# Optimization experiments

Measured on AMD Instinct MI355X. Metric: run time of the kernel, lower is better.

## Reference

```python
import jax, jax.numpy as jnp
import numpy as np

EMB = 256
N_NODES = 100000
N_EDGES = 500000
N_REL = 10
REL_DIM = 64
HID = 128
HEADS = 4
HEAD_DIM = HID // HEADS


def setup_inputs() -> dict:
    key = jax.random.key(0)
    ks = jax.random.split(key, 16)
    s = lambda i, shape: jax.random.normal(ks[i], shape, dtype=jnp.float32) * 0.05
    return {
        "node_embeddings": jax.random.normal(ks[0], (N_NODES, EMB), dtype=jnp.float32),
        "edge_index": jax.random.randint(ks[1], (2, N_EDGES), 0, N_NODES),
        "relation_type": jax.random.randint(ks[2], (N_EDGES,), 0, N_REL),
        "rel_emb": s(3, (N_REL, REL_DIM)),
        "W_edge": s(4, (2 * EMB, HID)), "b_edge": jnp.zeros((HID,), jnp.float32),
        "W_q": s(5, (REL_DIM, HID)), "b_q": jnp.zeros((HID,), jnp.float32),
        "W_k": s(6, (HID, HID)), "b_k": jnp.zeros((HID,), jnp.float32),
        "W_v": s(7, (HID, HID)), "b_v": jnp.zeros((HID,), jnp.float32),
        "W_o1": s(8, (HID, HID)), "b_o1": jnp.zeros((HID,), jnp.float32),
        "W_o2": s(9, (HID, 1)), "b_o2": jnp.zeros((1,), jnp.float32),
    }


def reference(node_embeddings, edge_index, relation_type, rel_emb,
              W_edge, b_edge, W_q, b_q, W_k, b_k, W_v, b_v,
              W_o1, b_o1, W_o2, b_o2):
    # Gather endpoint features: [E, 2*EMB]
    src = node_embeddings[edge_index[0]]
    tgt = node_embeddings[edge_index[1]]
    edge_features = jnp.concatenate([src, tgt], axis=1)
    # Edge MLP (dropout is identity at eval): [E, HID]
    edge_hidden = jax.nn.relu(edge_features @ W_edge + b_edge)
    # Relation embedding lookup: [E, REL_DIM]
    rel = rel_emb[relation_type]
    E = edge_hidden.shape[0]
    Q = (rel @ W_q + b_q).reshape(E, HEADS, HEAD_DIM)
    K = (edge_hidden @ W_k + b_k).reshape(E, HEADS, HEAD_DIM)
    V = (edge_hidden @ W_v + b_v).reshape(E, HEADS, HEAD_DIM)
    scale = jnp.sqrt(jnp.float32(HEAD_DIM))
    scores = jnp.sum(Q * K, axis=-1) / scale          # [E, HEADS]
    attn = jax.nn.softmax(scores, axis=-1)            # softmax over heads
    attended = (attn[..., None] * V).reshape(E, HID)
    output = attended + edge_hidden
    # Output MLP: Linear->ReLU->Linear(1)
    h = jax.nn.relu(output @ W_o1 + b_o1)
    score = (h @ W_o2 + b_o2).squeeze(-1)             # [E]
    return score
```

## Files before the change

kernel.cpp:

```cpp
#include <hip/hip_runtime.h>

#define EMB   256
#define HID   128
#define RELD  64
#define NREL  10
#define TE    64

typedef __attribute__((ext_vector_type(8)))  short bf16x8;
typedef __attribute__((ext_vector_type(16))) float f32x16;

__device__ __forceinline__ float bf16_to_f32(unsigned short u) {
    union { unsigned int i; float f; } v;
    v.i = ((unsigned int)u) << 16;
    return v.f;
}

__device__ __forceinline__ unsigned short f32_to_bf16(float x) {
    union { unsigned int i; float f; } v;
    v.f = x;
    unsigned int b = v.i;
    unsigned int rounded = b + 0x7fffu + ((b >> 16) & 1u);
    return (unsigned short)(rounded >> 16);
}

template <bool F32>
__device__ __forceinline__ float ldx(const void* p, size_t i) {
    if (F32) return ((const float*)p)[i];
    return bf16_to_f32(((const unsigned short*)p)[i]);
}

__device__ __forceinline__ bool detect_f32(const void* nodeEmb) {
    const float* f = (const float*)nodeEmb;
    float x = f[(threadIdx.x & 63) * 997];
    bool sane = isfinite(x) && fabsf(x) < 1.0e6f;
    unsigned long long m = __ballot(sane);
    return __popcll(m) >= 48;
}

template <bool F32>
__device__ void prep_body(const void* W_edge, const void* W_k, const void* W_v,
                          const void* W_o1, const void* rel_emb, const void* W_q,
                          const void* b_q,
                          unsigned short* WTe, unsigned short* WTk,
                          unsigned short* WTv, unsigned short* WTo1, float* Qtab)
{
    if (blockIdx.x < 448) {
        int idx = blockIdx.x * 256 + threadIdx.x;
        if (idx < 65536) {
            int col = idx >> 9, k = idx & 511;
            WTe[idx] = f32_to_bf16(ldx<F32>(W_edge, (size_t)k * HID + col));
        } else if (idx < 65536 + 16384) {
            int i = idx - 65536; int col = i >> 7, k = i & 127;
            WTk[i] = f32_to_bf16(ldx<F32>(W_k, (size_t)k * HID + col));
        } else if (idx < 65536 + 2 * 16384) {
            int i = idx - 65536 - 16384; int col = i >> 7, k = i & 127;
            WTv[i] = f32_to_bf16(ldx<F32>(W_v, (size_t)k * HID + col));
        } else {
            int i = idx - 65536 - 2 * 16384; int col = i >> 7, k = i & 127;
            WTo1[i] = f32_to_bf16(ldx<F32>(W_o1, (size_t)k * HID + col));
        }
    } else {
        const int t = threadIdx.x;
        const int c = t & (HID - 1);
        const int h = t >> 7;
        for (int r = h; r < NREL; r += 2) {
            float acc = 0.f;
            for (int d = 0; d < RELD; ++d)
                acc += ldx<F32>(rel_emb, r * RELD + d) * ldx<F32>(W_q, (size_t)d * HID + c);
            Qtab[r * HID + c] = acc + ldx<F32>(b_q, c);
        }
    }
}

__global__ void prep_kernel(const void* nodeEmb,
                            const void* W_edge, const void* W_k, const void* W_v,
                            const void* W_o1, const void* rel_emb, const void* W_q,
                            const void* b_q,
                            unsigned short* WTe, unsigned short* WTk,
                            unsigned short* WTv, unsigned short* WTo1, float* Qtab)
{
    if (detect_f32(nodeEmb))
        prep_body<true >(W_edge, W_k, W_v, W_o1, rel_emb, W_q, b_q,
                         WTe, WTk, WTv, WTo1, Qtab);
    else
        prep_body<false>(W_edge, W_k, W_v, W_o1, rel_emb, W_q, b_q,
                         WTe, WTk, WTv, WTo1, Qtab);
}

struct __align__(16) Smem {
    unsigned short sHid[TE][136];
    union {
        unsigned short sA[TE][40];
        float          sQf[NREL * HID];
    } u;
    unsigned short sB[HID][40];
    float sBias[5 * HID];
    float sSc[TE][4], sAttn[TE][4];
    float sPart[TE][2];
    int   sSrc[TE], sTgt[TE], sRel[TE];
};

__device__ __forceinline__ void gemm128(Smem& sm, const unsigned short* WT,
                                        f32x16* acc, int t, int rt, int cg2,
                                        int c, int h5)
{
    for (int kc = 0; kc < 4; ++kc) {
        #pragma unroll
        for (int j = 0; j < 2; ++j) {
            int g = t + j * 256;
            int col = g >> 2, gg = g & 3;
            *(uint4*)&sm.sB[col][gg * 8] =
                *(const uint4*)(WT + (size_t)col * HID + kc * 32 + gg * 8);
        }
        __syncthreads();
        #pragma unroll
        for (int s = 0; s < 2; ++s) {
            bf16x8 a = *(const bf16x8*)&sm.sHid[32 * rt + c][kc * 32 + s * 16 + h5 * 8];
            #pragma unroll
            for (int ct = 0; ct < 2; ++ct) {
                bf16x8 b = *(const bf16x8*)&sm.sB[64 * cg2 + 32 * ct + c][s * 16 + h5 * 8];
                acc[ct] = __builtin_amdgcn_mfma_f32_32x32x16_bf16(a, b, acc[ct], 0, 0, 0);
            }
        }
        __syncthreads();
    }
}

template <bool F32>
__device__ void fused_body(
    Smem& sm,
    const void* nodeEmb, const int* edgeIdx, const int* relType,
    const unsigned short* WTe, const unsigned short* WTk,
    const unsigned short* WTv, const unsigned short* WTo1,
    const void* b_edge, const void* b_k, const void* b_v,
    const void* b_o1, const void* W_o2, const void* b_o2,
    const float* Qtab, void* outp, int E)
{
    const int t   = threadIdx.x;
    const int l   = t & 63;
    const int w   = t >> 6;
    const int c   = l & 31;
    const int h5  = l >> 5;
    const int rt  = w & 1;
    const int cg2 = w >> 1;
    const int bs  = blockIdx.x * TE;

    if (t < TE) {
        int e = bs + t;
        if (e >= E) e = E - 1;
        if (e < 0)  e = 0;
        sm.sSrc[t] = edgeIdx[e];
        sm.sTgt[t] = edgeIdx[E + e];
        int r = relType[e];
        if (r < 0) r = 0;
        if (r >= NREL) r = NREL - 1;
        sm.sRel[t] = r;
    }
    for (int i = t; i < 5 * HID; i += 256) {
        int which = i >> 7, j = i & (HID - 1);
        float v = (which == 0) ? ldx<F32>(b_edge, j)
                : (which == 1) ? ldx<F32>(b_k, j)
                : (which == 2) ? ldx<F32>(b_v, j)
                : (which == 3) ? ldx<F32>(b_o1, j)
                               : ldx<F32>(W_o2, j);
        sm.sBias[i] = v;
    }
    __syncthreads();

    const int edge_s = t >> 2;
    const int grp    = t & 3;

    f32x16 acc[2];
    acc[0] = (f32x16)(0.0f); acc[1] = (f32x16)(0.0f);
    for (int kc = 0; kc < 16; ++kc) {
        {
            int node = (kc < 8) ? sm.sSrc[edge_s] : sm.sTgt[edge_s];
            int col0 = (kc & 7) * 32 + grp * 8;
            if (F32) {
                const float* p = (const float*)nodeEmb + (size_t)node * EMB + col0;
                float4 f0 = *(const float4*)p;
                float4 f1 = *(const float4*)(p + 4);
                union { unsigned short us[8]; uint4 v; } pk;
                pk.us[0] = f32_to_bf16(f0.x); pk.us[1] = f32_to_bf16(f0.y);
                pk.us[2] = f32_to_bf16(f0.z); pk.us[3] = f32_to_bf16(f0.w);
                pk.us[4] = f32_to_bf16(f1.x); pk.us[5] = f32_to_bf16(f1.y);
                pk.us[6] = f32_to_bf16(f1.z); pk.us[7] = f32_to_bf16(f1.w);
                *(uint4*)&sm.u.sA[edge_s][grp * 8] = pk.v;
            } else {
                *(uint4*)&sm.u.sA[edge_s][grp * 8] =
                    *(const uint4*)((const unsigned short*)nodeEmb +
                                    (size_t)node * EMB + col0);
            }
        }
        #pragma unroll
        for (int j = 0; j < 2; ++j) {
            int g = t + j * 256;
            int col = g >> 2, gg = g & 3;
            *(uint4*)&sm.sB[col][gg * 8] =
                *(const uint4*)(WTe + (size_t)col * 512 + kc * 32 + gg * 8);
        }
        __syncthreads();
        #pragma unroll
        for (int s = 0; s < 2; ++s) {
            bf16x8 a = *(const bf16x8*)&sm.u.sA[32 * rt + c][s * 16 + h5 * 8];
            #pragma unroll
            for (int ct = 0; ct < 2; ++ct) {
                bf16x8 b = *(const bf16x8*)&sm.sB[64 * cg2 + 32 * ct + c][s * 16 + h5 * 8];
                acc[ct] = __builtin_amdgcn_mfma_f32_32x32x16_bf16(a, b, acc[ct], 0, 0, 0);
            }
        }
        __syncthreads();
    }
    {
        #pragma unroll
        for (int ct = 0; ct < 2; ++ct) {
            int col = 64 * cg2 + 32 * ct + c;
            float bb = sm.sBias[col];
            #pragma unroll
            for (int r = 0; r < 16; ++r) {
                int erow = 32 * rt + (r & 3) + 8 * (r >> 2) + 4 * h5;
                sm.sHid[erow][col] = f32_to_bf16(fmaxf(acc[ct][r] + bb, 0.f));
            }
        }
    }
    __syncthreads();
    for (int i = t; i < NREL * HID; i += 256)
        sm.u.sQf[i] = Qtab[i];

    f32x16 kacc[2];
    kacc[0] = (f32x16)(0.0f); kacc[1] = (f32x16)(0.0f);
    gemm128(sm, WTk, kacc, t, rt, cg2, c, h5);

    {
        float ps[2][16];
        #pragma unroll
        for (int ct = 0; ct < 2; ++ct) {
            int col = 64 * cg2 + 32 * ct + c;
            float bk = sm.sBias[HID + col];
            #pragma unroll
            for (int r = 0; r < 16; ++r) {
                int erow = 32 * rt + (r & 3) + 8 * (r >> 2) + 4 * h5;
                ps[ct][r] = (kacc[ct][r] + bk) * sm.u.sQf[sm.sRel[erow] * HID + col];
            }
        }
        #pragma unroll
        for (int m = 1; m < 32; m <<= 1)
            #pragma unroll
            for (int ct = 0; ct < 2; ++ct)
                #pragma unroll
                for (int r = 0; r < 16; ++r)
                    ps[ct][r] += __shfl_xor(ps[ct][r], m, 64);
        if (c == 0) {
            const float inv = 0.17677669529663687f;
            #pragma unroll
            for (int ct = 0; ct < 2; ++ct) {
                int head = 2 * cg2 + ct;
                #pragma unroll
                for (int r = 0; r < 16; ++r) {
                    int erow = 32 * rt + (r & 3) + 8 * (r >> 2) + 4 * h5;
                    sm.sSc[erow][head] = ps[ct][r] * inv;
                }
            }
        }
    }
    __syncthreads();
    if (t < TE) {
        float s0 = sm.sSc[t][0], s1 = sm.sSc[t][1];
        float s2 = sm.sSc[t][2], s3 = sm.sSc[t][3];
        float m = fmaxf(fmaxf(s0, s1), fmaxf(s2, s3));
        float e0 = expf(s0 - m), e1 = expf(s1 - m);
        float e2 = expf(s2 - m), e3 = expf(s3 - m);
        float den = e0 + e1 + e2 + e3;
        sm.sAttn[t][0] = e0 / den; sm.sAttn[t][1] = e1 / den;
        sm.sAttn[t][2] = e2 / den; sm.sAttn[t][3] = e3 / den;
    }
    __syncthreads();

    f32x16 vacc[2];
    vacc[0] = (f32x16)(0.0f); vacc[1] = (f32x16)(0.0f);
    gemm128(sm, WTv, vacc, t, rt, cg2, c, h5);
    {
        #pragma unroll
        for (int ct = 0; ct < 2; ++ct) {
            int col  = 64 * cg2 + 32 * ct + c;
            int head = 2 * cg2 + ct;
            float bv = sm.sBias[2 * HID + col];
            #pragma unroll
            for (int r = 0; r < 16; ++r) {
                int erow = 32 * rt + (r & 3) + 8 * (r >> 2) + 4 * h5;
                float at = sm.sAttn[erow][head];
                float hv = bf16_to_f32(sm.sHid[erow][col]);
                sm.sHid[erow][col] = f32_to_bf16(at * (vacc[ct][r] + bv) + hv);
            }
        }
    }

    f32x16 oacc[2];
    oacc[0] = (f32x16)(0.0f); oacc[1] = (f32x16)(0.0f);
    gemm128(sm, WTo1, oacc, t, rt, cg2, c, h5);
    {
        float pr[16];
        #pragma unroll
        for (int r = 0; r < 16; ++r) pr[r] = 0.f;
        #pragma unroll
        for (int ct = 0; ct < 2; ++ct) {
            int col = 64 * cg2 + 32 * ct + c;
            float bo = sm.sBias[3 * HID + col];
            float wo = sm.sBias[4 * HID + col];
            #pragma unroll
            for (int r = 0; r < 16; ++r)
                pr[r] += fmaxf(oacc[ct][r] + bo, 0.f) * wo;
        }
        #pragma unroll
        for (int m = 1; m < 32; m <<= 1)
            #pragma unroll
            for (int r = 0; r < 16; ++r)
                pr[r] += __shfl_xor(pr[r], m, 64);
        if (c == 0) {
            #pragma unroll
            for (int r = 0; r < 16; ++r) {
                int erow = 32 * rt + (r & 3) + 8 * (r >> 2) + 4 * h5;
                sm.sPart[erow][cg2] = pr[r];
            }
        }
    }
    __syncthreads();
    if (t < TE) {
        int ge = bs + t;
        if (ge < E) {
            float val = sm.sPart[t][0] + sm.sPart[t][1] + ldx<F32>(b_o2, 0);
            if (F32) ((float*)outp)[ge] = val;
            else     ((unsigned short*)outp)[ge] = f32_to_bf16(val);
        }
    }
}

__global__ __launch_bounds__(256, 4) void RelationAttentionMLPHead_10539849744626_kernel(
    const void* nodeEmb, const int* edgeIdx, const int* relType,
    const unsigned short* WTe, const unsigned short* WTk,
    const unsigned short* WTv, const unsigned short* WTo1,
    const void* b_edge, const void* b_k, const void* b_v,
    const void* b_o1, const void* W_o2, const void* b_o2,
    const float* Qtab, void* outp, int E)
{
    __shared__ Smem sm;
    if (detect_f32(nodeEmb))
        fused_body<true >(sm, nodeEmb, edgeIdx, relType, WTe, WTk, WTv, WTo1,
                          b_edge, b_k, b_v, b_o1, W_o2, b_o2, Qtab, outp, E);
    else
        fused_body<false>(sm, nodeEmb, edgeIdx, relType, WTe, WTk, WTv, WTo1,
                          b_edge, b_k, b_v, b_o1, W_o2, b_o2, Qtab, outp, E);
}

extern "C" void kernel_launch(void* const* d_in, const int* in_sizes, int n_in,
                              void* d_out, int out_size, void* d_ws, size_t ws_size,
                              hipStream_t stream) {
    (void)n_in; (void)ws_size;

    const void* nodeEmb = d_in[0];
    const int*  edgeIdx = (const int*)d_in[1];
    const int*  relType = (const int*)d_in[2];
    const void* rel_emb = d_in[3];
    const void* W_edge  = d_in[4];
    const void* b_edge  = d_in[5];
    const void* W_q     = d_in[6];
    const void* b_q     = d_in[7];
    const void* W_k     = d_in[8];
    const void* b_k     = d_in[9];
    const void* W_v     = d_in[10];
    const void* b_v     = d_in[11];
    const void* W_o1    = d_in[12];
    const void* b_o1    = d_in[13];
    const void* W_o2    = d_in[14];
    const void* b_o2    = d_in[15];

    int E = out_size;
    if (E <= 0) E = in_sizes ? in_sizes[2] : 0;
    if (E <= 0) E = 500000;

    char* ws = (char*)d_ws;
    float*          Qtab = (float*)ws;
    unsigned short* WTe  = (unsigned short*)(ws + 8192);
    unsigned short* WTk  = (unsigned short*)(ws + 139264);
    unsigned short* WTv  = (unsigned short*)(ws + 172032);
    unsigned short* WTo1 = (unsigned short*)(ws + 204800);

    prep_kernel<<<449, 256, 0, stream>>>(nodeEmb, W_edge, W_k, W_v, W_o1,
                                         rel_emb, W_q, b_q,
                                         WTe, WTk, WTv, WTo1, Qtab);

    int grid = (E + TE - 1) / TE;
    if (grid < 1) grid = 1;

    RelationAttentionMLPHead_10539849744626_kernel<<<grid, 256, 0, stream>>>(
        nodeEmb, edgeIdx, relType, WTe, WTk, WTv, WTo1,
        b_edge, b_k, b_v, b_o1, W_o2, b_o2, Qtab, d_out, E);
}
```

Baseline: 472.1 us.

## Pre-convert node embeddings to bf16 and register-prefetch next GEMM tiles

Adds a conversion pass in the prep kernel that writes the fp32 node embedding table to a bf16 copy in the workspace. The fused kernel then gathers bf16 rows, halving gather bytes per edge. Global loads for the next A and B tiles now go into registers ahead of the MFMAs so they overlap compute, with one barrier per step instead of two. The weight tile in shared memory also gets a fragment-ordered layout. In exchange, the full 100k×256 table (about 100 MB read, 50 MB written) is converted on every call, and the bf16 path only runs if the workspace is large enough.

```diff
diff --git a/kernel.cpp b/kernel.cpp
--- a/kernel.cpp
+++ b/kernel.cpp
@@ -38,14 +38,14 @@
 }
 
 template <bool F32>
-__device__ void prep_body(const void* W_edge, const void* W_k, const void* W_v,
-                          const void* W_o1, const void* rel_emb, const void* W_q,
-                          const void* b_q,
+__device__ void prep_body(int vb, const void* W_edge, const void* W_k,
+                          const void* W_v, const void* W_o1, const void* rel_emb,
+                          const void* W_q, const void* b_q,
                           unsigned short* WTe, unsigned short* WTk,
                           unsigned short* WTv, unsigned short* WTo1, float* Qtab)
 {
-    if (blockIdx.x < 448) {
-        int idx = blockIdx.x * 256 + threadIdx.x;
+    if (vb < 448) {
+        int idx = vb * 256 + threadIdx.x;
         if (idx < 65536) {
             int col = idx >> 9, k = idx & 511;
             WTe[idx] = f32_to_bf16(ldx<F32>(W_edge, (size_t)k * HID + col));
@@ -77,23 +77,42 @@
                             const void* W_o1, const void* rel_emb, const void* W_q,
                             const void* b_q,
                             unsigned short* WTe, unsigned short* WTk,
-                            unsigned short* WTv, unsigned short* WTo1, float* Qtab)
+                            unsigned short* WTv, unsigned short* WTo1, float* Qtab,
+                            unsigned short* nodeBf16, int convBlocks,
+                            unsigned long long nodeElems)
 {
-    if (detect_f32(nodeEmb))
-        prep_body<true >(W_edge, W_k, W_v, W_o1, rel_emb, W_q, b_q,
-                         WTe, WTk, WTv, WTo1, Qtab);
-    else
-        prep_body<false>(W_edge, W_k, W_v, W_o1, rel_emb, W_q, b_q,
-                         WTe, WTk, WTv, WTo1, Qtab);
+    bool f32 = detect_f32(nodeEmb);
+    int b = blockIdx.x;
+    if (b < convBlocks) {
+        if (!f32) return;
+        unsigned long long i = (unsigned long long)b * 2048ull + threadIdx.x * 8;
+        if (i + 8 <= nodeElems) {
+            const float* src = (const float*)nodeEmb + i;
+            float4 f0 = *(const float4*)src;
+            float4 f1 = *(const float4*)(src + 4);
+            union { unsigned short us[8]; uint4 v; } pk;
+            pk.us[0] = f32_to_bf16(f0.x); pk.us[1] = f32_to_bf16(f0.y);
+            pk.us[2] = f32_to_bf16(f0.z); pk.us[3] = f32_to_bf16(f0.w);
+            pk.us[4] = f32_to_bf16(f1.x); pk.us[5] = f32_to_bf16(f1.y);
+            pk.us[6] = f32_to_bf16(f1.z); pk.us[7] = f32_to_bf16(f1.w);
+            *(uint4*)(nodeBf16 + i) = pk.v;
+        }
+        return;
+    }
+    b -= convBlocks;
+    if (f32) prep_body<true >(b, W_edge, W_k, W_v, W_o1, rel_emb, W_q, b_q,
+                              WTe, WTk, WTv, WTo1, Qtab);
+    else     prep_body<false>(b, W_edge, W_k, W_v, W_o1, rel_emb, W_q, b_q,
+                              WTe, WTk, WTv, WTo1, Qtab);
 }
 
 struct __align__(16) Smem {
     unsigned short sHid[TE][136];
     union {
         unsigned short sA[TE][40];
-        float          sQf[NREL * HID];
+        float sQf[NREL * HID];
     } u;
-    unsigned short sB[HID][40];
+    unsigned short sB[4096];
     float sBias[5 * HID];
     float sSc[TE][4], sAttn[TE][4];
     float sPart[TE][2];
@@ -101,35 +120,44 @@
 };
 
 __device__ __forceinline__ void gemm128(Smem& sm, const unsigned short* WT,
+                                        const unsigned short* WTnext,
                                         f32x16* acc, int t, int rt, int cg2,
-                                        int c, int h5)
+                                        int c, int h5, int l, uint4* pb)
 {
     for (int kc = 0; kc < 4; ++kc) {
+        __syncthreads();
         #pragma unroll
         for (int j = 0; j < 2; ++j) {
-            int g = t + j * 256;
-            int col = g >> 2, gg = g & 3;
-            *(uint4*)&sm.sB[col][gg * 8] =
-                *(const uint4*)(WT + (size_t)col * HID + kc * 32 + gg * 8);
+            int g = t + j * 256, col = g & 127, kg = g >> 7;
+            int uu = ((col >> 5) * 4 + kg) * 32 + (col & 31);
+            *(uint4*)&sm.sB[uu * 8] = pb[j];
         }
         __syncthreads();
+        const unsigned short* Wn = (kc < 3) ? WT : WTnext;
+        int kcn = (kc < 3) ? kc + 1 : 0;
+        if (Wn) {
+            #pragma unroll
+            for (int j = 0; j < 2; ++j) {
+                int g = t + j * 256, col = g & 127, kg = g >> 7;
+                pb[j] = *(const uint4*)(Wn + (size_t)col * HID + kcn * 32 + kg * 8);
+            }
+        }
         #pragma unroll
         for (int s = 0; s < 2; ++s) {
             bf16x8 a = *(const bf16x8*)&sm.sHid[32 * rt + c][kc * 32 + s * 16 + h5 * 8];
             #pragma unroll
             for (int ct = 0; ct < 2; ++ct) {
-                bf16x8 b = *(const bf16x8*)&sm.sB[64 * cg2 + 32 * ct + c][s * 16 + h5 * 8];
+                bf16x8 b = *(const bf16x8*)&sm.sB[((cg2 * 2 + ct) * 128 + s * 64 + l) * 8];
                 acc[ct] = __builtin_amdgcn_mfma_f32_32x32x16_bf16(a, b, acc[ct], 0, 0, 0);
             }
         }
-        __syncthreads();
-    }
-}
-
-template <bool F32>
+    }
+}
+
+template <bool F32, bool GBF16>
 __device__ void fused_body(
     Smem& sm,
-    const void* nodeEmb, const int* edgeIdx, const int* relType,
+    const void* gsrc, const int* edgeIdx, const int* relType,
     const unsigned short* WTe, const unsigned short* WTk,
     const unsigned short* WTv, const unsigned short* WTo1,
     const void* b_edge, const void* b_k, const void* b_v,
@@ -170,46 +198,78 @@
     const int edge_s = t >> 2;
     const int grp    = t & 3;
 
+    uint4  paU;
+    float4 paF0, paF1;
+    uint4  pb[2];
+
+    {
+        int node = sm.sSrc[edge_s];
+        int col0 = grp * 8;
+        if (GBF16) {
+            paU = *(const uint4*)((const unsigned short*)gsrc + (size_t)node * EMB + col0);
+        } else {
+            const float* p = (const float*)gsrc + (size_t)node * EMB + col0;
+            paF0 = *(const float4*)p; paF1 = *(const float4*)(p + 4);
+        }
+        #pragma unroll
+        for (int j = 0; j < 2; ++j) {
+            int g = t + j * 256, col = g & 127, kg = g >> 7;
+            pb[j] = *(const uint4*)(WTe + (size_t)col * 512 + kg * 8);
+        }
+    }
+
     f32x16 acc[2];
     acc[0] = (f32x16)(0.0f); acc[1] = (f32x16)(0.0f);
     for (int kc = 0; kc < 16; ++kc) {
-        {
-            int node = (kc < 8) ? sm.sSrc[edge_s] : sm.sTgt[edge_s];
-            int col0 = (kc & 7) * 32 + grp * 8;
-            if (F32) {
-                const float* p = (const float*)nodeEmb + (size_t)node * EMB + col0;
-                float4 f0 = *(const float4*)p;
-                float4 f1 = *(const float4*)(p + 4);
-                union { unsigned short us[8]; uint4 v; } pk;
-                pk.us[0] = f32_to_bf16(f0.x); pk.us[1] = f32_to_bf16(f0.y);
-                pk.us[2] = f32_to_bf16(f0.z); pk.us[3] = f32_to_bf16(f0.w);
-                pk.us[4] = f32_to_bf16(f1.x); pk.us[5] = f32_to_bf16(f1.y);
-                pk.us[6] = f32_to_bf16(f1.z); pk.us[7] = f32_to_bf16(f1.w);
-                *(uint4*)&sm.u.sA[edge_s][grp * 8] = pk.v;
+        __syncthreads();
+        if (GBF16) {
+            *(uint4*)&sm.u.sA[edge_s][grp * 8] = paU;
+        } else {
+            union { unsigned short us[8]; uint4 v; } pk;
+            pk.us[0] = f32_to_bf16(paF0.x); pk.us[1] = f32_to_bf16(paF0.y);
+            pk.us[2] = f32_to_bf16(paF0.z); pk.us[3] = f32_to_bf16(paF0.w);
+            pk.us[4] = f32_to_bf16(paF1.x); pk.us[5] = f32_to_bf16(paF1.y);
+            pk.us[6] = f32_to_bf16(paF1.z); pk.us[7] = f32_to_bf16(paF1.w);
+            *(uint4*)&sm.u.sA[edge_s][grp * 8] = pk.v;
+        }
+        #pragma unroll
+        for (int j = 0; j < 2; ++j) {
+            int g = t + j * 256, col = g & 127, kg = g >> 7;
+            int uu = ((col >> 5) * 4 + kg) * 32 + (col & 31);
+            *(uint4*)&sm.sB[uu * 8] = pb[j];
+        }
+        __syncthreads();
+        if (kc < 15) {
+            int kn = kc + 1;
+            int node = (kn < 8) ? sm.sSrc[edge_s] : sm.sTgt[edge_s];
+            int col0 = (kn & 7) * 32 + grp * 8;
+            if (GBF16) {
+                paU = *(const uint4*)((const unsigned short*)gsrc + (size_t)node * EMB + col0);
             } else {
-                *(uint4*)&sm.u.sA[edge_s][grp * 8] =
-                    *(const uint4*)((const unsigned short*)nodeEmb +
-                                    (size_t)node * EMB + col0);
-            }
-        }
-        #pragma unroll
-        for (int j = 0; j < 2; ++j) {
-            int g = t + j * 256;
-            int col = g >> 2, gg = g & 3;
-            *(uint4*)&sm.sB[col][gg * 8] =
-                *(const uint4*)(WTe + (size_t)col * 512 + kc * 32 + gg * 8);
-        }
-        __syncthreads();
+                const float* p = (const float*)gsrc + (size_t)node * EMB + col0;
+                paF0 = *(const float4*)p; paF1 = *(const float4*)(p + 4);
+            }
+            #pragma unroll
+            for (int j = 0; j < 2; ++j) {
+                int g = t + j * 256, col = g & 127, kg = g >> 7;
+                pb[j] = *(const uint4*)(WTe + (size_t)col * 512 + kn * 32 + kg * 8);
+            }
+        } else {
+            #pragma unroll
+            for (int j = 0; j < 2; ++j) {
+                int g = t + j * 256, col = g & 127, kg = g >> 7;
+                pb[j] = *(const uint4*)(WTk + (size_t)col * HID + kg * 8);
+            }
+        }
         #pragma unroll
         for (int s = 0; s < 2; ++s) {
             bf16x8 a = *(const bf16x8*)&sm.u.sA[32 * rt + c][s * 16 + h5 * 8];
             #pragma unroll
             for (int ct = 0; ct < 2; ++ct) {
-                bf16x8 b = *(const bf16x8*)&sm.sB[64 * cg2 + 32 * ct + c][s * 16 + h5 * 8];
+                bf16x8 b = *(const bf16x8*)&sm.sB[((cg2 * 2 + ct) * 128 + s * 64 + l) * 8];
                 acc[ct] = __builtin_amdgcn_mfma_f32_32x32x16_bf16(a, b, acc[ct], 0, 0, 0);
             }
         }
-        __syncthreads();
     }
     {
         #pragma unroll
@@ -229,7 +289,7 @@
 
     f32x16 kacc[2];
     kacc[0] = (f32x16)(0.0f); kacc[1] = (f32x16)(0.0f);
-    gemm128(sm, WTk, kacc, t, rt, cg2, c, h5);
+    gemm128(sm, WTk, WTv, kacc, t, rt, cg2, c, h5, l, pb);
 
     {
         float ps[2][16];
@@ -278,7 +338,7 @@
 
     f32x16 vacc[2];
     vacc[0] = (f32x16)(0.0f); vacc[1] = (f32x16)(0.0f);
-    gemm128(sm, WTv, vacc, t, rt, cg2, c, h5);
+    gemm128(sm, WTv, WTo1, vacc, t, rt, cg2, c, h5, l, pb);
     {
         #pragma unroll
         for (int ct = 0; ct < 2; ++ct) {
@@ -297,7 +357,7 @@
 
     f32x16 oacc[2];
     oacc[0] = (f32x16)(0.0f); oacc[1] = (f32x16)(0.0f);
-    gemm128(sm, WTo1, oacc, t, rt, cg2, c, h5);
+    gemm128(sm, WTo1, nullptr, oacc, t, rt, cg2, c, h5, l, pb);
     {
         float pr[16];
         #pragma unroll
@@ -336,7 +396,8 @@
 }
 
 __global__ __launch_bounds__(256, 4) void RelationAttentionMLPHead_10539849744626_kernel(
-    const void* nodeEmb, const int* edgeIdx, const int* relType,
+    const void* nodeEmb, const unsigned short* nodeBf16, int useConv,
+    const int* edgeIdx, const int* relType,
     const unsigned short* WTe, const unsigned short* WTk,
     const unsigned short* WTv, const unsigned short* WTo1,
     const void* b_edge, const void* b_k, const void* b_v,
@@ -344,18 +405,23 @@
     const float* Qtab, void* outp, int E)
 {
     __shared__ Smem sm;
-    if (detect_f32(nodeEmb))
-        fused_body<true >(sm, nodeEmb, edgeIdx, relType, WTe, WTk, WTv, WTo1,
-                          b_edge, b_k, b_v, b_o1, W_o2, b_o2, Qtab, outp, E);
-    else
-        fused_body<false>(sm, nodeEmb, edgeIdx, relType, WTe, WTk, WTv, WTo1,
-                          b_edge, b_k, b_v, b_o1, W_o2, b_o2, Qtab, outp, E);
+    if (detect_f32(nodeEmb)) {
+        if (useConv)
+            fused_body<true, true >(sm, nodeBf16, edgeIdx, relType, WTe, WTk, WTv, WTo1,
+                                    b_edge, b_k, b_v, b_o1, W_o2, b_o2, Qtab, outp, E);
+        else
+            fused_body<true, false>(sm, nodeEmb, edgeIdx, relType, WTe, WTk, WTv, WTo1,
+                                    b_edge, b_k, b_v, b_o1, W_o2, b_o2, Qtab, outp, E);
+    } else {
+        fused_body<false, true>(sm, nodeEmb, edgeIdx, relType, WTe, WTk, WTv, WTo1,
+                                b_edge, b_k, b_v, b_o1, W_o2, b_o2, Qtab, outp, E);
+    }
 }
 
 extern "C" void kernel_launch(void* const* d_in, const int* in_sizes, int n_in,
                               void* d_out, int out_size, void* d_ws, size_t ws_size,
                               hipStream_t stream) {
-    (void)n_in; (void)ws_size;
+    (void)n_in;
 
     const void* nodeEmb = d_in[0];
     const int*  edgeIdx = (const int*)d_in[1];
@@ -378,21 +444,29 @@
     if (E <= 0) E = in_sizes ? in_sizes[2] : 0;
     if (E <= 0) E = 500000;
 
+    unsigned long long nodeElems =
+        (in_sizes && in_sizes[0] > 0) ? (unsigned long long)in_sizes[0] : 25600000ull;
+
     char* ws = (char*)d_ws;
-    float*          Qtab = (float*)ws;
-    unsigned short* WTe  = (unsigned short*)(ws + 8192);
-    unsigned short* WTk  = (unsigned short*)(ws + 139264);
-    unsigned short* WTv  = (unsigned short*)(ws + 172032);
-    unsigned short* WTo1 = (unsigned short*)(ws + 204800);
-
-    prep_kernel<<<449, 256, 0, stream>>>(nodeEmb, W_edge, W_k, W_v, W_o1,
-                                         rel_emb, W_q, b_q,
-                                         WTe, WTk, WTv, WTo1, Qtab);
+    float*          Qtab     = (float*)ws;
+    unsigned short* WTe      = (unsigned short*)(ws + 8192);
+    unsigned short* WTk      = (unsigned short*)(ws + 139264);
+    unsigned short* WTv      = (unsigned short*)(ws + 172032);
+    unsigned short* WTo1     = (unsigned short*)(ws + 204800);
+    unsigned short* nodeBf16 = (unsigned short*)(ws + 237568);
+
+    size_t need = 237568ull + nodeElems * 2ull;
+    int useConv = (ws_size >= need) ? 1 : 0;
+    int convBlocks = useConv ? (int)((nodeElems + 2047ull) / 2048ull) : 0;
+
+    prep_kernel<<<convBlocks + 449, 256, 0, stream>>>(
+        nodeEmb, W_edge, W_k, W_v, W_o1, rel_emb, W_q, b_q,
+        WTe, WTk, WTv, WTo1, Qtab, nodeBf16, convBlocks, nodeElems);
 
     int grid = (E + TE - 1) / TE;
     if (grid < 1) grid = 1;
 
     RelationAttentionMLPHead_10539849744626_kernel<<<grid, 256, 0, stream>>>(
-        nodeEmb, edgeIdx, relType, WTe, WTk, WTv, WTo1,
+        nodeEmb, nodeBf16, useConv, edgeIdx, relType, WTe, WTk, WTv, WTo1,
         b_edge, b_k, b_v, b_o1, W_o2, b_o2, Qtab, d_out, E);
 }
```

New measurement: 759.7 us. 60.9% more time.
